# Optimization experiments

Hardware: AMD Instinct MI355X
Metric: run time of the kernel (lower is better)

## Reference

```python
import jax, jax.numpy as jnp
import numpy as np

D_MODEL = 512
N_HEADS = 8
D_K = 64
B, T = 64, 256


def setup_inputs() -> dict:
    key = jax.random.key(0)
    ks = jax.random.split(key, 5)
    x = jax.random.normal(ks[0], (B, T, D_MODEL), dtype=jnp.float32)
    s = 1.0 / np.sqrt(D_MODEL)
    Wq = jax.random.normal(ks[1], (N_HEADS, D_MODEL, D_K), dtype=jnp.float32) * s
    Wk = jax.random.normal(ks[2], (N_HEADS, D_MODEL, D_K), dtype=jnp.float32) * s
    Wv = jax.random.normal(ks[3], (N_HEADS, D_MODEL, D_K), dtype=jnp.float32) * s
    Wo = jax.random.normal(ks[4], (N_HEADS * D_K, D_MODEL), dtype=jnp.float32) * s
    return {"x": x, "Wq": Wq, "Wk": Wk, "Wv": Wv, "Wo": Wo}


def reference(x, Wq, Wk, Wv, Wo):
    Bc, Tc, C = x.shape  # C == d_model; source scales by C**0.5, not sqrt(d_k)
    q = jnp.einsum('btc,hcd->bhtd', x, Wq)
    k = jnp.einsum('btc,hcd->bhtd', x, Wk)
    v = jnp.einsum('btc,hcd->bhtd', x, Wv)
    scores = jnp.einsum('bhtd,bhsd->bhts', q, k) / jnp.sqrt(jnp.float32(C))
    causal = jnp.tril(jnp.ones((Tc, Tc), dtype=bool))
    scores = jnp.where(causal, scores, -jnp.inf)
    attn = jax.nn.softmax(scores, axis=-1)  # dropout = identity in eval mode
    out = jnp.einsum('bhts,bhsd->bhtd', attn, v)
    out = out.transpose(0, 2, 1, 3).reshape(Bc, Tc, -1)  # concat heads
    return out @ Wo  # final dropout = identity in eval mode
```

## Files before the change

kernel.cpp:

```cpp
#include <hip/hip_runtime.h>
#include <hip/hip_bf16.h>

typedef __attribute__((ext_vector_type(4))) float f32x4;
typedef __attribute__((ext_vector_type(8))) short bf16x8;
typedef __attribute__((ext_vector_type(4))) short s16x4;
typedef __attribute__((ext_vector_type(4))) unsigned int u32x4;

#define DEV static __device__ __forceinline__

DEV unsigned short f2b(float f) {
  union { float f; unsigned int u; } v; v.f = f;
  unsigned int u = v.u;
  return (unsigned short)((u + 0x7fffu + ((u >> 16) & 1u)) >> 16);
}

DEV void gll16(const void* g, void* l) {
  __builtin_amdgcn_global_load_lds((__attribute__((address_space(1))) void*)g,
                                   (__attribute__((address_space(3))) void*)l,
                                   16, 0, 0);
}

__global__ __launch_bounds__(256) void prep(const float* __restrict__ x,
                                            const float* __restrict__ Wq,
                                            const float* __restrict__ Wk,
                                            const float* __restrict__ Wv,
                                            const float* __restrict__ Wo,
                                            unsigned short* __restrict__ xb,
                                            unsigned short* __restrict__ Wt,
                                            unsigned short* __restrict__ WoT) {
  const int bid = blockIdx.x;
  if (bid < 8192) {
    int id = bid * 256 + threadIdx.x;
    f32x4 v = *(const f32x4*)(x + (long)id * 4);
    s16x4 o;
    o.x = (short)f2b(v.x); o.y = (short)f2b(v.y);
    o.z = (short)f2b(v.z); o.w = (short)f2b(v.w);
    *(s16x4*)(xb + (long)id * 4) = o;
    return;
  }

  __shared__ unsigned int L[64 * 65];
  const int tx = threadIdx.x & 63;
  const int ty = threadIdx.x >> 6;

  int tb = bid - 8192;
  if (tb < 192) {
    int proj = tb >> 6, h = (tb >> 3) & 7, c0 = (tb & 7) << 6;
    const float* W = (proj == 0) ? Wq : ((proj == 1) ? Wk : Wv);
    const float* base = W + (long)h * 32768 + (long)c0 * 64;
#pragma unroll
    for (int i = 0; i < 16; i++) {
      int c = ty + i * 4;
      L[tx * 65 + c] = f2b(base[(long)c * 64 + tx]);
    }
    __syncthreads();
    unsigned short* out = Wt + ((long)(proj * 512 + h * 64)) * 512 + c0;
#pragma unroll
    for (int i = 0; i < 16; i++) {
      int d = ty + i * 4;
      out[(long)d * 512 + tx] = (unsigned short)L[d * 65 + tx];
    }
  } else {
    int t = tb - 192;
    int n0 = (t >> 3) << 6, c0 = (t & 7) << 6;
#pragma unroll
    for (int i = 0; i < 16; i++) {
      int c = ty + i * 4;
      L[tx * 65 + c] = f2b(Wo[(long)(c0 + c) * 512 + n0 + tx]);
    }
    __syncthreads();
    unsigned short* out = WoT + (long)n0 * 512 + c0;
#pragma unroll
    for (int i = 0; i < 16; i++) {
      int n = ty + i * 4;
      out[(long)n * 512 + tx] = (unsigned short)L[n * 65 + tx];
    }
  }
}

template <int F32OUT>
__global__ __launch_bounds__(256, 2) void gemm_bt(const unsigned short* __restrict__ A,
                                                  const unsigned short* __restrict__ BT,
                                                  void* __restrict__ Cv,
                                                  int N) {
  const int K = 512;
  __shared__ unsigned short As[128 * 64];
  __shared__ unsigned short Bs[128 * 64];

  const int tid = threadIdx.x;
  const int wave = tid >> 6, lane = tid & 63;
  const int quad = lane >> 4, l16 = lane & 15;
  const int wm = wave >> 1, wn = wave & 1;

  const int NB = N >> 7;
  const int nwg = gridDim.x;
  const int q = nwg >> 3, r = nwg & 7;
  const int xcd = blockIdx.x & 7, ci = blockIdx.x >> 3;
  const int wg = (xcd < r ? xcd * (q + 1) : r * (q + 1) + (xcd - r) * q) + ci;
  const int bn = wg % NB;
  const int bm = wg / NB;

  const int srow = lane >> 3;
  const int scol = ((lane & 7) ^ srow) * 8;

  f32x4 acc[4][4] = {};

  for (int kk = 0; kk < K; kk += 64) {
    __syncthreads();
#pragma unroll
    for (int s = 0; s < 4; s++) {
      int seg = wave * 4 + s;
      int row = seg * 8 + srow;
      gll16(A + (long)(bm * 128 + row) * K + kk + scol, As + seg * 512);
      gll16(BT + (long)(bn * 128 + row) * K + kk + scol, Bs + seg * 512);
    }
    __syncthreads();

#pragma unroll
    for (int kc = 0; kc < 2; kc++) {
      const int rq = (((kc * 4 + quad) ^ (l16 & 7)) * 8);
      bf16x8 af[4], bfv[4];
#pragma unroll
      for (int mt = 0; mt < 4; mt++)
        af[mt] = *(const bf16x8*)(As + (wm * 64 + mt * 16 + l16) * 64 + rq);
#pragma unroll
      for (int nt = 0; nt < 4; nt++)
        bfv[nt] = *(const bf16x8*)(Bs + (wn * 64 + nt * 16 + l16) * 64 + rq);
#pragma unroll
      for (int mt = 0; mt < 4; mt++)
#pragma unroll
        for (int nt = 0; nt < 4; nt++)
          acc[mt][nt] = __builtin_amdgcn_mfma_f32_16x16x32_bf16(af[mt], bfv[nt], acc[mt][nt], 0, 0, 0);
    }
  }

#pragma unroll
  for (int mt = 0; mt < 4; mt++) {
#pragma unroll
    for (int nt = 0; nt < 4; nt++) {
      int row0 = bm * 128 + wm * 64 + mt * 16 + quad * 4;
      int col = bn * 128 + wn * 64 + nt * 16 + l16;
      if (F32OUT) {
        float* cp = (float*)Cv + (long)row0 * N + col;
#pragma unroll
        for (int r2 = 0; r2 < 4; r2++)
          cp[(long)r2 * N] = acc[mt][nt][r2];
      } else {
        unsigned short* cp = (unsigned short*)Cv + (long)row0 * N + col;
#pragma unroll
        for (int r2 = 0; r2 < 4; r2++)
          cp[(long)r2 * N] = f2b(acc[mt][nt][r2]);
      }
    }
  }
}

__global__ __launch_bounds__(256, 2) void attn(const unsigned short* __restrict__ QKV,
                                               unsigned short* __restrict__ AO) {
  const int bh = blockIdx.x;
  const int b = bh >> 3, h = bh & 7;
  const int tid = threadIdx.x;
  const int wave = tid >> 6, lane = tid & 63;
  const int quad = lane >> 4, l16 = lane & 15;

  __shared__ unsigned short Kl[256 * 64];
  __shared__ unsigned short Vt[64 * 264];
  __shared__ unsigned short Pl[4][32 * 40];

  const unsigned short* Qb = QKV + (long)b * 256 * 1536 + h * 64;
  const unsigned short* Kb = Qb + 512;
  const unsigned short* Vb = Qb + 1024;

  {
    int r = lane >> 3, cg = lane & 7;
#pragma unroll
    for (int s = 0; s < 8; s++) {
      int seg = wave * 8 + s;
      gll16(Kb + (long)(seg * 8 + r) * 1536 + ((cg ^ r) * 8), Kl + seg * 512);
    }
  }
  {
    int j = tid;
    const unsigned short* vp = Vb + (long)j * 1536;
#pragma unroll
    for (int g = 0; g < 8; g++) {
      union { u32x4 v; unsigned short s[8]; } d;
      d.v = *(const u32x4*)(vp + g * 8);
#pragma unroll
      for (int q = 0; q < 8; q++)
        Vt[(g * 8 + q) * 264 + j] = d.s[q];
    }
  }
  const int tiles[2] = {wave, 7 - wave};
  bf16x8 qf[2][2][2];
#pragma unroll
  for (int ti = 0; ti < 2; ti++)
#pragma unroll
    for (int kc = 0; kc < 2; kc++)
#pragma unroll
      for (int mt = 0; mt < 2; mt++)
        qf[ti][kc][mt] = *(const bf16x8*)(Qb +
            (long)(tiles[ti] * 32 + mt * 16 + l16) * 1536 + kc * 32 + quad * 8);

  __syncthreads();

  f32x4 O[2][2][4] = {};
  float lsum[2][2][4] = {};
  const float scale = 0.044194173824159216f;

#pragma unroll
  for (int ti = 0; ti < 2; ti++) {
    const int t = tiles[ti];
    for (int c32 = 0; c32 <= t; c32++) {
      f32x4 S[2][2] = {};
#pragma unroll
      for (int kc = 0; kc < 2; kc++) {
        bf16x8 kbf[2];
#pragma unroll
        for (int st = 0; st < 2; st++) {
          int jrow = c32 * 32 + st * 16 + l16;
          kbf[st] = *(const bf16x8*)(Kl + jrow * 64 + (((kc * 4 + quad) ^ (jrow & 7)) * 8));
        }
#pragma unroll
        for (int mt = 0; mt < 2; mt++)
#pragma unroll
          for (int st = 0; st < 2; st++)
            S[mt][st] = __builtin_amdgcn_mfma_f32_16x16x32_bf16(qf[ti][kc][mt], kbf[st], S[mt][st], 0, 0, 0);
      }
      const bool diag = (c32 == t);
#pragma unroll
      for (int mt = 0; mt < 2; mt++)
#pragma unroll
        for (int st = 0; st < 2; st++)
#pragma unroll
          for (int r = 0; r < 4; r++) {
            int trow = mt * 16 + quad * 4 + r;
            float p = __expf(S[mt][st][r] * scale);
            if (diag && (st * 16 + l16 > trow)) p = 0.0f;
            lsum[ti][mt][r] += p;
            Pl[wave][trow * 40 + st * 16 + l16] = f2b(p);
          }
      bf16x8 pa[2], vbf[4];
#pragma unroll
      for (int mt = 0; mt < 2; mt++)
        pa[mt] = *(const bf16x8*)(&Pl[wave][(mt * 16 + l16) * 40 + quad * 8]);
#pragma unroll
      for (int dt = 0; dt < 4; dt++)
        vbf[dt] = *(const bf16x8*)(Vt + (dt * 16 + l16) * 264 + c32 * 32 + quad * 8);
#pragma unroll
      for (int mt = 0; mt < 2; mt++)
#pragma unroll
        for (int dt = 0; dt < 4; dt++)
          O[ti][mt][dt] = __builtin_amdgcn_mfma_f32_16x16x32_bf16(pa[mt], vbf[dt], O[ti][mt][dt], 0, 0, 0);
    }
  }

  float linv[2][2][4];
#pragma unroll
  for (int ti = 0; ti < 2; ti++)
#pragma unroll
    for (int mt = 0; mt < 2; mt++)
#pragma unroll
      for (int r = 0; r < 4; r++) {
        float s = lsum[ti][mt][r];
        s += __shfl_xor(s, 1); s += __shfl_xor(s, 2);
        s += __shfl_xor(s, 4); s += __shfl_xor(s, 8);
        linv[ti][mt][r] = 1.0f / s;
      }
#pragma unroll
  for (int ti = 0; ti < 2; ti++)
#pragma unroll
    for (int mt = 0; mt < 2; mt++)
#pragma unroll
      for (int dt = 0; dt < 4; dt++)
#pragma unroll
        for (int r = 0; r < 4; r++) {
          int t_ = tiles[ti] * 32 + mt * 16 + quad * 4 + r;
          int d = dt * 16 + l16;
          AO[(long)(b * 256 + t_) * 512 + h * 64 + d] = f2b(O[ti][mt][dt][r] * linv[ti][mt][r]);
        }
}

extern "C" void kernel_launch(void* const* d_in, const int* in_sizes, int n_in,
                              void* d_out, int out_size, void* d_ws, size_t ws_size,
                              hipStream_t stream) {
  const float* x  = (const float*)d_in[0];
  const float* Wq = (const float*)d_in[1];
  const float* Wk = (const float*)d_in[2];
  const float* Wv = (const float*)d_in[3];
  const float* Wo = (const float*)d_in[4];

  unsigned short* Wt  = (unsigned short*)d_ws;
  unsigned short* WoT = Wt + 1536 * 512;
  unsigned short* xb  = WoT + 512 * 512;
  unsigned short* QKV = xb + (long)16384 * 512;
  unsigned short* AO  = QKV + (long)16384 * 1536;
  float* out = (float*)d_out;

  prep<<<8448, 256, 0, stream>>>(x, Wq, Wk, Wv, Wo, xb, Wt, WoT);

  gemm_bt<0><<<1536, 256, 0, stream>>>(xb, Wt, (void*)QKV, 1536);

  attn<<<512, 256, 0, stream>>>(QKV, AO);

  gemm_bt<1><<<512, 256, 0, stream>>>(AO, WoT, (void*)out, 512);
}
```

Measured before the change: 156.7 us.

## Fuse fp32-to-bf16 input conversion into QKV GEMM with double-buffered LDS

The separate pass that converted x to bf16 is removed. The QKV GEMM now loads fp32 A tiles into registers, converts them to bf16 and writes them swizzled into LDS. The B tiles keep using direct global-to-LDS loads. Both operands are double-buffered, so the next tile's loads overlap the MFMA work on the current tile. This avoids a full write and re-read of the bf16 activation buffer and one kernel's traffic, but it doubles global A bytes per tile, raises register use, and uses 64KB of LDS per block.

After: 171.5 us. +9.5%, slower.

```diff
diff --git a/kernel.cpp b/kernel.cpp
--- a/kernel.cpp
+++ b/kernel.cpp
@@ -20,30 +20,17 @@
                                    16, 0, 0);
 }
 
-__global__ __launch_bounds__(256) void prep(const float* __restrict__ x,
-                                            const float* __restrict__ Wq,
+__global__ __launch_bounds__(256) void prep(const float* __restrict__ Wq,
                                             const float* __restrict__ Wk,
                                             const float* __restrict__ Wv,
                                             const float* __restrict__ Wo,
-                                            unsigned short* __restrict__ xb,
                                             unsigned short* __restrict__ Wt,
                                             unsigned short* __restrict__ WoT) {
-  const int bid = blockIdx.x;
-  if (bid < 8192) {
-    int id = bid * 256 + threadIdx.x;
-    f32x4 v = *(const f32x4*)(x + (long)id * 4);
-    s16x4 o;
-    o.x = (short)f2b(v.x); o.y = (short)f2b(v.y);
-    o.z = (short)f2b(v.z); o.w = (short)f2b(v.w);
-    *(s16x4*)(xb + (long)id * 4) = o;
-    return;
-  }
-
   __shared__ unsigned int L[64 * 65];
   const int tx = threadIdx.x & 63;
   const int ty = threadIdx.x >> 6;
 
-  int tb = bid - 8192;
+  int tb = blockIdx.x;
   if (tb < 192) {
     int proj = tb >> 6, h = (tb >> 3) & 7, c0 = (tb & 7) << 6;
     const float* W = (proj == 0) ? Wq : ((proj == 1) ? Wk : Wv);
@@ -78,14 +65,15 @@
   }
 }
 
-template <int F32OUT>
-__global__ __launch_bounds__(256, 2) void gemm_bt(const unsigned short* __restrict__ A,
+template <int F32A, int F32OUT>
+__global__ __launch_bounds__(256, 2) void gemm_bt(const void* __restrict__ Av,
                                                   const unsigned short* __restrict__ BT,
                                                   void* __restrict__ Cv,
                                                   int N) {
   const int K = 512;
-  __shared__ unsigned short As[128 * 64];
-  __shared__ unsigned short Bs[128 * 64];
+  __shared__ unsigned short sm[4 * 128 * 64];
+  unsigned short* const Asb[2] = {sm, sm + 8192};
+  unsigned short* const Bsb[2] = {sm + 16384, sm + 24576};
 
   const int tid = threadIdx.x;
   const int wave = tid >> 6, lane = tid & 63;
@@ -100,38 +88,97 @@
   const int bn = wg % NB;
   const int bm = wg / NB;
 
+  const float* Af = (const float*)Av;
+  const unsigned short* Ab = (const unsigned short*)Av;
+
   const int srow = lane >> 3;
   const int scol = ((lane & 7) ^ srow) * 8;
 
   f32x4 acc[4][4] = {};
 
-  for (int kk = 0; kk < K; kk += 64) {
-    __syncthreads();
+  f32x4 rawA[8];
+  u32x4 prA[4];
+
+  auto loadA = [&](int t) {
+#pragma unroll
+    for (int r4 = 0; r4 < 4; r4++) {
+      int ar = r4 * 32 + (tid >> 3), ac = tid & 7;
+      long off = (long)(bm * 128 + ar) * K + t * 64 + ac * 8;
+      if (F32A) {
+        rawA[r4 * 2]     = *(const f32x4*)(Af + off);
+        rawA[r4 * 2 + 1] = *(const f32x4*)(Af + off + 4);
+      } else {
+        prA[r4] = *(const u32x4*)(Ab + off);
+      }
+    }
+  };
+  auto cvtA = [&]() {
+    if (F32A) {
+#pragma unroll
+      for (int r4 = 0; r4 < 4; r4++) {
+        f32x4 lo = rawA[r4 * 2], hi = rawA[r4 * 2 + 1];
+        u32x4 w;
+        w.x = (unsigned)f2b(lo.x) | ((unsigned)f2b(lo.y) << 16);
+        w.y = (unsigned)f2b(lo.z) | ((unsigned)f2b(lo.w) << 16);
+        w.z = (unsigned)f2b(hi.x) | ((unsigned)f2b(hi.y) << 16);
+        w.w = (unsigned)f2b(hi.z) | ((unsigned)f2b(hi.w) << 16);
+        prA[r4] = w;
+      }
+    }
+  };
+  auto writeA = [&](unsigned short* buf) {
+#pragma unroll
+    for (int r4 = 0; r4 < 4; r4++) {
+      int ar = r4 * 32 + (tid >> 3), ac = tid & 7;
+      *(u32x4*)(buf + ar * 64 + ((ac ^ (ar & 7)) * 8)) = prA[r4];
+    }
+  };
+  auto stageB = [&](int t, unsigned short* buf) {
 #pragma unroll
     for (int s = 0; s < 4; s++) {
       int seg = wave * 4 + s;
       int row = seg * 8 + srow;
-      gll16(A + (long)(bm * 128 + row) * K + kk + scol, As + seg * 512);
-      gll16(BT + (long)(bn * 128 + row) * K + kk + scol, Bs + seg * 512);
-    }
-    __syncthreads();
-
+      gll16(BT + (long)(bn * 128 + row) * K + t * 64 + scol, buf + seg * 512);
+    }
+  };
+  auto compute = [&](const unsigned short* Ac, const unsigned short* Bc) {
 #pragma unroll
     for (int kc = 0; kc < 2; kc++) {
       const int rq = (((kc * 4 + quad) ^ (l16 & 7)) * 8);
       bf16x8 af[4], bfv[4];
 #pragma unroll
       for (int mt = 0; mt < 4; mt++)
-        af[mt] = *(const bf16x8*)(As + (wm * 64 + mt * 16 + l16) * 64 + rq);
+        af[mt] = *(const bf16x8*)(Ac + (wm * 64 + mt * 16 + l16) * 64 + rq);
 #pragma unroll
       for (int nt = 0; nt < 4; nt++)
-        bfv[nt] = *(const bf16x8*)(Bs + (wn * 64 + nt * 16 + l16) * 64 + rq);
+        bfv[nt] = *(const bf16x8*)(Bc + (wn * 64 + nt * 16 + l16) * 64 + rq);
 #pragma unroll
       for (int mt = 0; mt < 4; mt++)
 #pragma unroll
         for (int nt = 0; nt < 4; nt++)
           acc[mt][nt] = __builtin_amdgcn_mfma_f32_16x16x32_bf16(af[mt], bfv[nt], acc[mt][nt], 0, 0, 0);
     }
+  };
+
+  loadA(0);
+  cvtA();
+  writeA(Asb[0]);
+  stageB(0, Bsb[0]);
+
+#pragma unroll
+  for (int t = 0; t < 8; t++) {
+    const unsigned short* Ac = Asb[t & 1];
+    const unsigned short* Bc = Bsb[t & 1];
+    unsigned short* An = Asb[(t & 1) ^ 1];
+    unsigned short* Bn = Bsb[(t & 1) ^ 1];
+    __syncthreads();
+    if (t < 7) {
+      loadA(t + 1);
+      stageB(t + 1, Bn);
+      cvtA();
+    }
+    compute(Ac, Bc);
+    if (t < 7) writeA(An);
   }
 
 #pragma unroll
@@ -292,16 +339,15 @@
 
   unsigned short* Wt  = (unsigned short*)d_ws;
   unsigned short* WoT = Wt + 1536 * 512;
-  unsigned short* xb  = WoT + 512 * 512;
-  unsigned short* QKV = xb + (long)16384 * 512;
+  unsigned short* QKV = WoT + 512 * 512;
   unsigned short* AO  = QKV + (long)16384 * 1536;
   float* out = (float*)d_out;
 
-  prep<<<8448, 256, 0, stream>>>(x, Wq, Wk, Wv, Wo, xb, Wt, WoT);
-
-  gemm_bt<0><<<1536, 256, 0, stream>>>(xb, Wt, (void*)QKV, 1536);
+  prep<<<256, 256, 0, stream>>>(Wq, Wk, Wv, Wo, Wt, WoT);
+
+  gemm_bt<1, 0><<<1536, 256, 0, stream>>>(x, Wt, (void*)QKV, 1536);
 
   attn<<<512, 256, 0, stream>>>(QKV, AO);
 
-  gemm_bt<1><<<512, 256, 0, stream>>>(AO, WoT, (void*)out, 512);
-}
+  gemm_bt<0, 1><<<512, 256, 0, stream>>>(AO, WoT, (void*)out, 512);
+}
```

## Triple-buffer GEMM K-loop with async LDS prefetch and explicit vmcnt waits

Applied to the files above, without the earlier changes.

Rewrites the bf16 GEMM main loop to use a three-stage LDS ring with K-step 32, issuing global-to-LDS loads two tiles ahead. Explicit s_waitcnt vmcnt counts and raw s_barriers replace the paired __syncthreads, so tile loads overlap with MFMA compute. The LDS swizzle is changed to fit 32-wide rows, and launch bounds are raised to target three blocks per CU. This adds more barriers per K element and relies on hand-counted outstanding loads being correct.

Result: slower. 161.9 us (+3.3%).

```diff
diff --git a/kernel.cpp b/kernel.cpp
--- a/kernel.cpp
+++ b/kernel.cpp
@@ -79,13 +79,13 @@
 }
 
 template <int F32OUT>
-__global__ __launch_bounds__(256, 2) void gemm_bt(const unsigned short* __restrict__ A,
+__global__ __launch_bounds__(256, 3) void gemm_bt(const unsigned short* __restrict__ A,
                                                   const unsigned short* __restrict__ BT,
                                                   void* __restrict__ Cv,
                                                   int N) {
   const int K = 512;
-  __shared__ unsigned short As[128 * 64];
-  __shared__ unsigned short Bs[128 * 64];
+  __shared__ unsigned short As[3][128 * 32];
+  __shared__ unsigned short Bs[3][128 * 32];
 
   const int tid = threadIdx.x;
   const int wave = tid >> 6, lane = tid & 63;
@@ -100,38 +100,55 @@
   const int bn = wg % NB;
   const int bm = wg / NB;
 
-  const int srow = lane >> 3;
-  const int scol = ((lane & 7) ^ srow) * 8;
+  const int srow = lane >> 2;
+  const int scg = lane & 3;
 
   f32x4 acc[4][4] = {};
 
-  for (int kk = 0; kk < K; kk += 64) {
-    __syncthreads();
-#pragma unroll
-    for (int s = 0; s < 4; s++) {
-      int seg = wave * 4 + s;
-      int row = seg * 8 + srow;
-      gll16(A + (long)(bm * 128 + row) * K + kk + scol, As + seg * 512);
-      gll16(BT + (long)(bn * 128 + row) * K + kk + scol, Bs + seg * 512);
-    }
-    __syncthreads();
-
-#pragma unroll
-    for (int kc = 0; kc < 2; kc++) {
-      const int rq = (((kc * 4 + quad) ^ (l16 & 7)) * 8);
-      bf16x8 af[4], bfv[4];
-#pragma unroll
-      for (int mt = 0; mt < 4; mt++)
-        af[mt] = *(const bf16x8*)(As + (wm * 64 + mt * 16 + l16) * 64 + rq);
+  auto stage = [&](int t, int buf) {
+#pragma unroll
+    for (int i = 0; i < 2; i++) {
+      int seg = wave * 2 + i;
+      int rr = seg * 16 + srow;
+      int gc = (scg ^ ((rr >> 1) & 3)) * 8;
+      gll16(A + (long)(bm * 128 + rr) * K + t * 32 + gc, &As[buf][seg * 512]);
+      gll16(BT + (long)(bn * 128 + rr) * K + t * 32 + gc, &Bs[buf][seg * 512]);
+    }
+  };
+
+  auto compute = [&](int buf) {
+    bf16x8 af[4], bfv[4];
+#pragma unroll
+    for (int mt = 0; mt < 4; mt++) {
+      int rr = wm * 64 + mt * 16 + l16;
+      af[mt] = *(const bf16x8*)(&As[buf][rr * 32 + ((quad ^ ((rr >> 1) & 3)) * 8)]);
+    }
+#pragma unroll
+    for (int nt = 0; nt < 4; nt++) {
+      int rr = wn * 64 + nt * 16 + l16;
+      bfv[nt] = *(const bf16x8*)(&Bs[buf][rr * 32 + ((quad ^ ((rr >> 1) & 3)) * 8)]);
+    }
+#pragma unroll
+    for (int mt = 0; mt < 4; mt++)
 #pragma unroll
       for (int nt = 0; nt < 4; nt++)
-        bfv[nt] = *(const bf16x8*)(Bs + (wn * 64 + nt * 16 + l16) * 64 + rq);
-#pragma unroll
-      for (int mt = 0; mt < 4; mt++)
-#pragma unroll
-        for (int nt = 0; nt < 4; nt++)
-          acc[mt][nt] = __builtin_amdgcn_mfma_f32_16x16x32_bf16(af[mt], bfv[nt], acc[mt][nt], 0, 0, 0);
-    }
+        acc[mt][nt] = __builtin_amdgcn_mfma_f32_16x16x32_bf16(af[mt], bfv[nt], acc[mt][nt], 0, 0, 0);
+  };
+
+  stage(0, 0);
+  stage(1, 1);
+
+#pragma unroll
+  for (int t = 0; t < 16; t++) {
+    if (t + 2 < 16) stage(t + 2, (t + 2) % 3);
+    if (t < 14)       asm volatile("s_waitcnt vmcnt(8)" ::: "memory");
+    else if (t == 14) asm volatile("s_waitcnt vmcnt(4)" ::: "memory");
+    else              asm volatile("s_waitcnt vmcnt(0)" ::: "memory");
+    __builtin_amdgcn_s_barrier();
+    __builtin_amdgcn_sched_barrier(0);
+    compute(t % 3);
+    __builtin_amdgcn_sched_barrier(0);
+    __builtin_amdgcn_s_barrier();
   }
 
 #pragma unroll
```

## Double-buffer LDS tiles in bf16 GEMM to overlap global loads with MFMA

Applied to the files above, without the earlier changes.

The GEMM kernel now keeps two LDS buffers for the A and B tiles. It issues the async global-to-LDS loads for the next K-step before computing on the current one, and uses explicit waitcnt and barrier calls in place of two __syncthreads per iteration. This aims to hide global memory latency behind the MFMA work. LDS use doubles to 64KB per block, which may limit the two-blocks-per-CU occupancy target.

Result: no change. 156.3 us (-0.3%).

```diff
diff --git a/kernel.cpp b/kernel.cpp
--- a/kernel.cpp
+++ b/kernel.cpp
@@ -84,8 +84,8 @@
                                                   void* __restrict__ Cv,
                                                   int N) {
   const int K = 512;
-  __shared__ unsigned short As[128 * 64];
-  __shared__ unsigned short Bs[128 * 64];
+  __shared__ unsigned short As[2][128 * 64];
+  __shared__ unsigned short Bs[2][128 * 64];
 
   const int tid = threadIdx.x;
   const int wave = tid >> 6, lane = tid & 63;
@@ -105,32 +105,51 @@
 
   f32x4 acc[4][4] = {};
 
-  for (int kk = 0; kk < K; kk += 64) {
-    __syncthreads();
+  auto stage = [&](int kk, int buf) {
 #pragma unroll
     for (int s = 0; s < 4; s++) {
       int seg = wave * 4 + s;
       int row = seg * 8 + srow;
-      gll16(A + (long)(bm * 128 + row) * K + kk + scol, As + seg * 512);
-      gll16(BT + (long)(bn * 128 + row) * K + kk + scol, Bs + seg * 512);
-    }
-    __syncthreads();
-
+      gll16(A + (long)(bm * 128 + row) * K + kk + scol, &As[buf][seg * 512]);
+      gll16(BT + (long)(bn * 128 + row) * K + kk + scol, &Bs[buf][seg * 512]);
+    }
+  };
+
+  auto compute = [&](int buf) {
 #pragma unroll
     for (int kc = 0; kc < 2; kc++) {
       const int rq = (((kc * 4 + quad) ^ (l16 & 7)) * 8);
       bf16x8 af[4], bfv[4];
 #pragma unroll
       for (int mt = 0; mt < 4; mt++)
-        af[mt] = *(const bf16x8*)(As + (wm * 64 + mt * 16 + l16) * 64 + rq);
+        af[mt] = *(const bf16x8*)(&As[buf][(wm * 64 + mt * 16 + l16) * 64 + rq]);
 #pragma unroll
       for (int nt = 0; nt < 4; nt++)
-        bfv[nt] = *(const bf16x8*)(Bs + (wn * 64 + nt * 16 + l16) * 64 + rq);
+        bfv[nt] = *(const bf16x8*)(&Bs[buf][(wn * 64 + nt * 16 + l16) * 64 + rq]);
 #pragma unroll
       for (int mt = 0; mt < 4; mt++)
 #pragma unroll
         for (int nt = 0; nt < 4; nt++)
           acc[mt][nt] = __builtin_amdgcn_mfma_f32_16x16x32_bf16(af[mt], bfv[nt], acc[mt][nt], 0, 0, 0);
+    }
+  };
+
+  stage(0, 0);
+  asm volatile("s_waitcnt vmcnt(0)" ::: "memory");
+  __builtin_amdgcn_s_barrier();
+  __builtin_amdgcn_sched_barrier(0);
+
+  int cur = 0;
+#pragma unroll
+  for (int t = 0; t < 8; t++) {
+    if (t < 7) stage((t + 1) * 64, cur ^ 1);
+    __builtin_amdgcn_sched_barrier(0);
+    compute(cur);
+    if (t < 7) {
+      asm volatile("s_waitcnt vmcnt(0)" ::: "memory");
+      __builtin_amdgcn_s_barrier();
+      __builtin_amdgcn_sched_barrier(0);
+      cur ^= 1;
     }
   }
 
```
